# Performance work log

Hardware: AMD Instinct MI355X
Metric: run time of the kernel (lower is better)

Reference implementation:

```python
import jax, jax.numpy as jnp
import numpy as np

DT_MIN, DT_MAX = 1e-3, 0.1
DT_RANK, D_STATE, D_CONV = 64, 16, 4


def setup_inputs() -> dict:
    key = jax.random.key(0)
    ks = jax.random.split(key, 8)
    B, T, Dm = 4, 4096, 1024
    Dn = 2 * Dm  # expand * d_model
    s = lambda k, shape, scale=0.02: (jax.random.normal(k, shape, jnp.float32) * scale)
    return {
        "x": jax.random.normal(ks[0], (B, T, Dm), jnp.float32),
        "W_in": s(ks[1], (2 * Dn, Dm)),
        "conv_w": s(ks[2], (Dn, 1, D_CONV), 0.1),
        "conv_b": jnp.zeros((Dn,), jnp.float32),
        "W_x": s(ks[3], (DT_RANK + 2 * D_STATE, Dn)),
        "W_dt": s(ks[4], (Dn, DT_RANK)),
        "b_dt": jnp.zeros((Dn,), jnp.float32),
        "log_A": jax.random.uniform(ks[5], (Dn, D_STATE), jnp.float32),
        "D_param": jnp.ones((Dn,), jnp.float32),
        "W_out": s(ks[6], (Dm, Dn)),
        "ln_w": jnp.ones((Dm,), jnp.float32),
        "ln_b": jnp.zeros((Dm,), jnp.float32),
    }


def reference(x, W_in, conv_w, conv_b, W_x, W_dt, b_dt, log_A, D_param, W_out, ln_w, ln_b):
    B, T, Dm = x.shape
    Dn = W_dt.shape[0]
    residual = x
    # LayerNorm (biased variance, eps=1e-5, as torch)
    mu = x.mean(-1, keepdims=True)
    var = x.var(-1, keepdims=True)
    xn = (x - mu) / jnp.sqrt(var + 1e-5) * ln_w + ln_b
    # in_proj -> split into x_inner, z
    xz = xn @ W_in.T  # (B,T,2*Dn)
    x_inner, z = jnp.split(xz, 2, axis=-1)
    # causal depthwise conv (torch pads both sides d_conv-1 then slices [:T] == left-pad only)
    xc = jnp.transpose(x_inner, (0, 2, 1))  # (B,Dn,T)
    xc = jax.lax.conv_general_dilated(
        xc, conv_w, window_strides=(1,), padding=[(D_CONV - 1, 0)],
        dimension_numbers=("NCH", "OIH", "NCH"), feature_group_count=Dn)
    xc = xc + conv_b[None, :, None]
    u = jax.nn.silu(jnp.transpose(xc, (0, 2, 1)))  # (B,T,Dn)
    # input-dependent dt, B, C
    xbc = u @ W_x.T
    dt_low, B_ssm, C_ssm = jnp.split(xbc, [DT_RANK, DT_RANK + D_STATE], axis=-1)
    dt = jax.nn.softplus(dt_low @ W_dt.T + b_dt) + DT_MIN
    dt = jnp.clip(dt, DT_MIN, DT_MAX)  # (B,T,Dn)
    A = -jnp.exp(log_A)  # (Dn,N), always negative -> stable
    # selective scan: h_t = exp(dt*A)*h_{t-1} + (dt*u)*B_t ; y_t = <C_t, h_t>
    def step(h, inp):
        dt_t, u_t, B_t, C_t = inp  # (B,Dn),(B,Dn),(B,N),(B,N)
        dA = jnp.exp(dt_t[:, :, None] * A)  # (B,Dn,N)
        h = dA * h + (dt_t * u_t)[:, :, None] * B_t[:, None, :]
        y = jnp.einsum("bdn,bn->bd", h, C_t)
        return h, y

    h0 = jnp.zeros((B, Dn, D_STATE), x.dtype)
    _, ys = jax.lax.scan(
        step, h0,
        (jnp.moveaxis(dt, 1, 0), jnp.moveaxis(u, 1, 0),
         jnp.moveaxis(B_ssm, 1, 0), jnp.moveaxis(C_ssm, 1, 0)))
    y = jnp.moveaxis(ys, 0, 1)  # (B,T,Dn)
    y = y + u * D_param
    y = y * jax.nn.silu(z)
    return y @ W_out.T + residual
```

## Files before the change

kernel.cpp:

```cpp
#include <hip/hip_runtime.h>
#include <cstdint>
#include <cstddef>

#define TT 4096
#define DM 1024
#define DN 2048
#define MROWS 16384
#define NCH 64
#define CHL 64
#define SW 16
#define XBCS 128

typedef unsigned short u16;
typedef u16 ushort8_t __attribute__((ext_vector_type(8)));
typedef u16 ushort4_t __attribute__((ext_vector_type(4)));
typedef short bf16x8 __attribute__((ext_vector_type(8)));
typedef float f32x4 __attribute__((ext_vector_type(4)));

#define EXP2(x) __builtin_amdgcn_exp2f(x)
#define L2E 1.44269504f

__device__ __forceinline__ float bf2f(u16 b) {
  return __uint_as_float(((unsigned int)b) << 16);
}
__device__ __forceinline__ u16 f2bf(float f) {
  unsigned int u = __float_as_uint(f);
  u = u + 0x7FFFu + ((u >> 16) & 1u);
  return (u16)(u >> 16);
}
__device__ __forceinline__ u16 f2h(float f) {
  _Float16 h = (_Float16)f;
  return __builtin_bit_cast(u16, h);
}
__device__ __forceinline__ float h2f(u16 v) {
  return (float)__builtin_bit_cast(_Float16, v);
}

__device__ __forceinline__ void gload_lds16(const void* g, void* l) {
  __builtin_amdgcn_global_load_lds(
      (const __attribute__((address_space(1))) unsigned int*)g,
      (__attribute__((address_space(3))) unsigned int*)l, 16, 0, 0);
}

__global__ __launch_bounds__(256) void cvt_bf16_kernel(const float* __restrict__ in,
    u16* __restrict__ out, int n4) {
  int i = blockIdx.x * 256 + threadIdx.x;
  if (i >= n4) return;
  float4 v = ((const float4*)in)[i];
  ushort4_t o; o[0] = f2bf(v.x); o[1] = f2bf(v.y); o[2] = f2bf(v.z); o[3] = f2bf(v.w);
  ((ushort4_t*)out)[i] = o;
}

__global__ __launch_bounds__(256) void cvt_wx_kernel(const float* __restrict__ W_x,
    u16* __restrict__ out) {
  int i = blockIdx.x * 256 + threadIdx.x;
  int row = i >> 9;
  ushort4_t o;
  if (row < 96) {
    float4 v = ((const float4*)W_x)[i];
    o[0] = f2bf(v.x); o[1] = f2bf(v.y); o[2] = f2bf(v.z); o[3] = f2bf(v.w);
  } else {
    o[0] = 0; o[1] = 0; o[2] = 0; o[3] = 0;
  }
  ((ushort4_t*)out)[i] = o;
}

__global__ __launch_bounds__(256) void ln_kernel(const float* __restrict__ x,
    const float* __restrict__ ln_w, const float* __restrict__ ln_b,
    u16* __restrict__ xn) {
  int row = blockIdx.x;
  int tid = threadIdx.x;
  const float4* xr = (const float4*)(x + (size_t)row * DM);
  float4 v = xr[tid];
  float s  = v.x + v.y + v.z + v.w;
  float s2 = v.x*v.x + v.y*v.y + v.z*v.z + v.w*v.w;
#pragma unroll
  for (int o = 32; o > 0; o >>= 1) { s += __shfl_down(s, o, 64); s2 += __shfl_down(s2, o, 64); }
  __shared__ float red[2][4];
  __shared__ float mv[2];
  int wid = tid >> 6, lane = tid & 63;
  if (lane == 0) { red[0][wid] = s; red[1][wid] = s2; }
  __syncthreads();
  if (tid == 0) {
    float a  = red[0][0] + red[0][1] + red[0][2] + red[0][3];
    float b2 = red[1][0] + red[1][1] + red[1][2] + red[1][3];
    float mean = a * (1.f / DM);
    float var  = b2 * (1.f / DM) - mean * mean;
    mv[0] = mean; mv[1] = rsqrtf(var + 1e-5f);
  }
  __syncthreads();
  float mean = mv[0], inv = mv[1];
  float4 w = ((const float4*)ln_w)[tid];
  float4 b = ((const float4*)ln_b)[tid];
  ushort4_t o;
  o[0] = f2bf((v.x - mean) * inv * w.x + b.x);
  o[1] = f2bf((v.y - mean) * inv * w.y + b.y);
  o[2] = f2bf((v.z - mean) * inv * w.z + b.z);
  o[3] = f2bf((v.w - mean) * inv * w.w + b.w);
  *(ushort4_t*)(xn + (size_t)row * DM + tid * 4) = o;
}

template<int MODE>
__global__ __launch_bounds__(256) void gemm_mfma_nt(
    const u16* __restrict__ A, int lda,
    const u16* __restrict__ B, int ldb,
    void* __restrict__ Cp, int ldc,
    const float* __restrict__ Res, int K,
    const float* __restrict__ bias, u16* __restrict__ dl_out) {
  __shared__ __align__(16) u16 a_s[128 * 64];
  __shared__ __align__(16) u16 b_s[128 * 64];
  const int tid = threadIdx.x;
  const int w = tid >> 6, l = tid & 63;
  const int wr = w >> 1, wc = w & 1;
  const int nbx = gridDim.x, gy = gridDim.y;
  int lin = blockIdx.y * nbx + blockIdx.x;
  int xcd = lin & 7;
  int m   = lin >> 3;
  int bi, bj;
  if (gy >= 8) {
    int njx = gy >> 3;
    bi = m / njx;
    bj = xcd * njx + m % njx;
  } else {
    int cpx = (nbx * gy) >> 3;
    int swz = xcd * cpx + m;
    bi = swz % nbx; bj = swz / nbx;
  }
  const int lrow = l >> 3;
  const int scol = ((l & 7) ^ lrow) * 16;

  f32x4 acc[4][4] = {};

  const u16* Abase = A + (size_t)(bi * 128 + w * 8 + lrow) * lda;
  const u16* Bbase = B + (size_t)(bj * 128 + w * 8 + lrow) * ldb;

  for (int k0 = 0; k0 < K; k0 += 64) {
#pragma unroll
    for (int c = 0; c < 4; c++) {
      const char* ga = (const char*)(Abase + (size_t)(c * 32) * lda + k0) + scol;
      const char* gb = (const char*)(Bbase + (size_t)(c * 32) * ldb + k0) + scol;
      gload_lds16(ga, (char*)a_s + c * 4096 + w * 1024);
      gload_lds16(gb, (char*)b_s + c * 4096 + w * 1024);
    }
    __syncthreads();
#pragma unroll
    for (int kk = 0; kk < 2; kk++) {
      bf16x8 af[4], bfr[4];
#pragma unroll
      for (int m2 = 0; m2 < 4; m2++) {
        int fr = wr * 64 + m2 * 16 + (l & 15);
        int cb = (kk * 64 + ((l >> 4) << 4)) ^ ((fr & 7) << 4);
        af[m2] = *(const bf16x8*)((const char*)a_s + fr * 128 + cb);
      }
#pragma unroll
      for (int n = 0; n < 4; n++) {
        int fr = wc * 64 + n * 16 + (l & 15);
        int cb = (kk * 64 + ((l >> 4) << 4)) ^ ((fr & 7) << 4);
        bfr[n] = *(const bf16x8*)((const char*)b_s + fr * 128 + cb);
      }
#pragma unroll
      for (int m2 = 0; m2 < 4; m2++)
#pragma unroll
        for (int n = 0; n < 4; n++)
          acc[m2][n] = __builtin_amdgcn_mfma_f32_16x16x32_bf16(af[m2], bfr[n], acc[m2][n], 0, 0, 0);
    }
    __syncthreads();
  }
  const int col0 = bj * 128 + wc * 64 + (l & 15);
  const int row0 = bi * 128 + wr * 64 + (l >> 4) * 4;
#pragma unroll
  for (int m2 = 0; m2 < 4; m2++)
#pragma unroll
    for (int n = 0; n < 4; n++) {
      int col = col0 + n * 16;
      float bv = 0.f;
      if constexpr (MODE == 3) bv = bias[col];
#pragma unroll
      for (int r = 0; r < 4; r++) {
        size_t row = (size_t)(row0 + m2 * 16 + r);
        float v = acc[m2][n][r];
        if constexpr (MODE == 0) {
          ((u16*)Cp)[row * ldc + col] = f2bf(v);
        } else if constexpr (MODE == 1) {
          ((float*)Cp)[row * ldc + col] = v;
          if (col < 64) dl_out[row * 64 + col] = f2bf(v);
        } else if constexpr (MODE == 2) {
          v += Res[row * ldc + col];
          ((float*)Cp)[row * ldc + col] = v;
        } else {
          float s = v + bv;
          float sp = __logf(1.f + __expf(s));
          float dtv = fminf(sp + 1e-3f, 0.1f);
          ((u16*)Cp)[row * ldc + col] = f2h(dtv);
        }
      }
    }
}

__global__ __launch_bounds__(256) void conv_silu_kernel(const u16* __restrict__ xz,
    const float* __restrict__ conv_w, const float* __restrict__ conv_b,
    u16* __restrict__ u) {
  size_t gid = (size_t)blockIdx.x * 256 + threadIdx.x;
  int c = (int)(gid & 255);
  size_t i = gid >> 8;
  int t = (int)(i & (TT - 1));
  int d0 = c * 8;
  const u16* base = xz + i * 4096 + d0;
  ushort8_t r0 = *(const ushort8_t*)base;
  ushort8_t r1 = 0, r2 = 0, r3 = 0;
  if (t >= 1) r1 = *(const ushort8_t*)(base - 4096);
  if (t >= 2) r2 = *(const ushort8_t*)(base - 2 * 4096);
  if (t >= 3) r3 = *(const ushort8_t*)(base - 3 * 4096);
  float cbv[8];
  *(float4*)&cbv[0] = *(const float4*)(conv_b + d0);
  *(float4*)&cbv[4] = *(const float4*)(conv_b + d0 + 4);
  ushort8_t o;
#pragma unroll
  for (int j = 0; j < 8; j++) {
    float4 w = *(const float4*)(conv_w + (size_t)(d0 + j) * 4);
    float a = cbv[j] + w.w * bf2f(r0[j]) + w.z * bf2f(r1[j])
            + w.y * bf2f(r2[j]) + w.x * bf2f(r3[j]);
    a = a * __builtin_amdgcn_rcpf(1.f + EXP2(-a * L2E));
    o[j] = f2bf(a);
  }
  *(ushort8_t*)(u + i * 2048 + d0) = o;
}

__global__ __launch_bounds__(256) void scan_part1(u16* u_g,
    const u16* __restrict__ dt_g, const float* __restrict__ xbc,
    const float* __restrict__ log_A, const float* __restrict__ D_param,
    float* __restrict__ hbuf, float* __restrict__ Sbuf) {
  int d0 = blockIdx.x * 128;
  int c  = blockIdx.y;
  int b  = blockIdx.z;
  int tid = threadIdx.x;
  int w = tid >> 6, l = tid & 63;
  int dl = tid >> 1, q = tid & 1, q8 = q << 3;
  int d = d0 + dl;
  __shared__ __align__(16) u16 u_s[2][SW][128];
  __shared__ __align__(16) u16 dts[2][SW][128];
  __shared__ __align__(16) float bc_s[2][SW][32];

  float A2[8];
  {
    float4 la0 = *(const float4*)(log_A + (size_t)d * 16 + q8);
    float4 la1 = *(const float4*)(log_A + (size_t)d * 16 + q8 + 4);
    A2[0] = -EXP2(la0.x * L2E) * L2E; A2[1] = -EXP2(la0.y * L2E) * L2E;
    A2[2] = -EXP2(la0.z * L2E) * L2E; A2[3] = -EXP2(la0.w * L2E) * L2E;
    A2[4] = -EXP2(la1.x * L2E) * L2E; A2[5] = -EXP2(la1.y * L2E) * L2E;
    A2[6] = -EXP2(la1.z * L2E) * L2E; A2[7] = -EXP2(la1.w * L2E) * L2E;
  }
  float Dp = D_param[d];
  float h[8] = {};
  float sdt = 0.f;
  size_t t0 = (size_t)b * TT + (size_t)c * CHL;
  const int sr = w * 4 + (l >> 4);
  const int sc = (l & 15) * 8;
  u16* up = u_g + t0 * 2048 + d;

#define P1STAGE(wnd, pb) { size_t i0_ = t0 + (size_t)(wnd) * SW;                          \
    gload_lds16(u_g  + (i0_ + sr) * 2048 + d0 + sc, (char*)u_s[pb] + w * 1024);           \
    gload_lds16(dt_g + (i0_ + sr) * 4096 + d0 + sc, (char*)dts[pb] + w * 1024);           \
    if (w < 2) gload_lds16(xbc + (i0_ + w * 8 + (l >> 3)) * XBCS + 64 + (l & 7) * 4,      \
                           (char*)bc_s[pb] + w * 1024); }

  P1STAGE(0, 0);
  for (int wnd = 0; wnd < CHL / SW; wnd++) {
    int pb = wnd & 1;
    __syncthreads();
    if (wnd + 1 < CHL / SW) P1STAGE(wnd + 1, pb ^ 1);
#pragma unroll 4
    for (int tt = 0; tt < SW; tt++) {
      float dtv = h2f(dts[pb][tt][dl]);
      float uv  = bf2f(u_s[pb][tt][dl]);
      sdt += dtv;
      float xin = dtv * uv;
      float yv = q ? 0.f : uv * Dp;
      float4 B0 = *(const float4*)&bc_s[pb][tt][q8];
      float4 B1 = *(const float4*)&bc_s[pb][tt][q8 + 4];
      float4 C0 = *(const float4*)&bc_s[pb][tt][16 + q8];
      float4 C1 = *(const float4*)&bc_s[pb][tt][16 + q8 + 4];
      h[0] = __builtin_fmaf(EXP2(dtv * A2[0]), h[0], xin * B0.x); yv = __builtin_fmaf(h[0], C0.x, yv);
      h[1] = __builtin_fmaf(EXP2(dtv * A2[1]), h[1], xin * B0.y); yv = __builtin_fmaf(h[1], C0.y, yv);
      h[2] = __builtin_fmaf(EXP2(dtv * A2[2]), h[2], xin * B0.z); yv = __builtin_fmaf(h[2], C0.z, yv);
      h[3] = __builtin_fmaf(EXP2(dtv * A2[3]), h[3], xin * B0.w); yv = __builtin_fmaf(h[3], C0.w, yv);
      h[4] = __builtin_fmaf(EXP2(dtv * A2[4]), h[4], xin * B1.x); yv = __builtin_fmaf(h[4], C1.x, yv);
      h[5] = __builtin_fmaf(EXP2(dtv * A2[5]), h[5], xin * B1.y); yv = __builtin_fmaf(h[5], C1.y, yv);
      h[6] = __builtin_fmaf(EXP2(dtv * A2[6]), h[6], xin * B1.z); yv = __builtin_fmaf(h[6], C1.z, yv);
      h[7] = __builtin_fmaf(EXP2(dtv * A2[7]), h[7], xin * B1.w); yv = __builtin_fmaf(h[7], C1.w, yv);
      yv += __shfl_xor(yv, 1, 64);
      if (q == 0) *up = f2h(yv);
      up += 2048;
    }
  }
  float* hp = hbuf + (((size_t)b * NCH + c) * 16 + q8) * DN + d;
#pragma unroll
  for (int k = 0; k < 8; k++) hp[(size_t)k * DN] = h[k];
  if (q == 0) Sbuf[((size_t)b * NCH + c) * DN + d] = sdt;
#undef P1STAGE
}

__global__ __launch_bounds__(256) void scan_combine(const float* __restrict__ log_A,
    const float* __restrict__ Sbuf, float* __restrict__ hbuf) {
  int idx = blockIdx.x * 256 + threadIdx.x;
  int dd = idx & (DN - 1), n = (idx >> 11) & 15, b = idx >> 15;
  float A2 = -EXP2(log_A[(size_t)dd * 16 + n] * L2E) * L2E;
  float h = 0.f;
#pragma unroll
  for (int c = 0; c < NCH; c++) {
    size_t off = (((size_t)b * NCH + c) * 16 + n) * DN + dd;
    float hl = hbuf[off];
    float P = EXP2(A2 * Sbuf[((size_t)b * NCH + c) * DN + dd]);
    hbuf[off] = h;
    h = hl + P * h;
  }
}

__global__ __launch_bounds__(256) void scan_part2(u16* yl,
    const u16* __restrict__ xz, const float* __restrict__ xbc,
    const u16* __restrict__ dt_g, const float* __restrict__ log_A,
    const float* __restrict__ hbuf) {
  int d0 = blockIdx.x * 128;
  int c  = blockIdx.y;
  int b  = blockIdx.z;
  int tid = threadIdx.x;
  int w = tid >> 6, l = tid & 63;
  int dl = tid >> 1, q = tid & 1, q8 = q << 3;
  int d = d0 + dl;
  __shared__ __align__(16) u16 yls[2][SW][128];
  __shared__ __align__(16) u16 z_s[2][SW][128];
  __shared__ __align__(16) u16 dts[2][SW][128];
  __shared__ __align__(16) float c_s[2][SW][16];

  float A2[8];
  {
    float4 la0 = *(const float4*)(log_A + (size_t)d * 16 + q8);
    float4 la1 = *(const float4*)(log_A + (size_t)d * 16 + q8 + 4);
    A2[0] = -EXP2(la0.x * L2E) * L2E; A2[1] = -EXP2(la0.y * L2E) * L2E;
    A2[2] = -EXP2(la0.z * L2E) * L2E; A2[3] = -EXP2(la0.w * L2E) * L2E;
    A2[4] = -EXP2(la1.x * L2E) * L2E; A2[5] = -EXP2(la1.y * L2E) * L2E;
    A2[6] = -EXP2(la1.z * L2E) * L2E; A2[7] = -EXP2(la1.w * L2E) * L2E;
  }
  float hs[8];
  {
    const float* hp = hbuf + (((size_t)b * NCH + c) * 16 + q8) * DN + d;
#pragma unroll
    for (int k = 0; k < 8; k++) hs[k] = hp[(size_t)k * DN];
  }
  float cum = 0.f;
  size_t t0 = (size_t)b * TT + (size_t)c * CHL;
  const int sr = w * 4 + (l >> 4);
  const int sc = (l & 15) * 8;
  u16* ylp = yl + t0 * 2048 + d;

#define P2STAGE(wnd, pb) { size_t i0_ = t0 + (size_t)(wnd) * SW;                          \
    gload_lds16(yl   + (i0_ + sr) * 2048 + d0 + sc, (char*)yls[pb] + w * 1024);           \
    gload_lds16(xz   + (i0_ + sr) * 4096 + 2048 + d0 + sc, (char*)z_s[pb] + w * 1024);    \
    gload_lds16(dt_g + (i0_ + sr) * 4096 + d0 + sc, (char*)dts[pb] + w * 1024);           \
    if (w == 0) gload_lds16(xbc + (i0_ + (l >> 2)) * XBCS + 80 + (l & 3) * 4,             \
                            (char*)c_s[pb]); }

  P2STAGE(0, 0);
  for (int wnd = 0; wnd < CHL / SW; wnd++) {
    int pb = wnd & 1;
    __syncthreads();
    if (wnd + 1 < CHL / SW) P2STAGE(wnd + 1, pb ^ 1);
#pragma unroll 4
    for (int tt = 0; tt < SW; tt++) {
      float dtv = h2f(dts[pb][tt][dl]);
      cum += dtv;
      float4 C0 = *(const float4*)&c_s[pb][tt][q8];
      float4 C1 = *(const float4*)&c_s[pb][tt][q8 + 4];
      float yv = C0.x * (EXP2(cum * A2[0]) * hs[0]) + C0.y * (EXP2(cum * A2[1]) * hs[1])
               + C0.z * (EXP2(cum * A2[2]) * hs[2]) + C0.w * (EXP2(cum * A2[3]) * hs[3])
               + C1.x * (EXP2(cum * A2[4]) * hs[4]) + C1.y * (EXP2(cum * A2[5]) * hs[5])
               + C1.z * (EXP2(cum * A2[6]) * hs[6]) + C1.w * (EXP2(cum * A2[7]) * hs[7]);
      if (q == 0) yv += h2f(yls[pb][tt][dl]);
      yv += __shfl_xor(yv, 1, 64);
      float zv = bf2f(z_s[pb][tt][dl]);
      float sig = __builtin_amdgcn_rcpf(1.f + EXP2(-zv * L2E));
      if (q == 0) *ylp = f2bf(yv * zv * sig);
      ylp += 2048;
    }
  }
#undef P2STAGE
}

extern "C" void kernel_launch(void* const* d_in, const int* in_sizes, int n_in,
                              void* d_out, int out_size, void* d_ws, size_t ws_size,
                              hipStream_t stream) {
  const float* x       = (const float*)d_in[0];
  const float* W_in    = (const float*)d_in[1];
  const float* conv_w  = (const float*)d_in[2];
  const float* conv_b  = (const float*)d_in[3];
  const float* W_x     = (const float*)d_in[4];
  const float* W_dt    = (const float*)d_in[5];
  const float* b_dt    = (const float*)d_in[6];
  const float* log_A   = (const float*)d_in[7];
  const float* D_param = (const float*)d_in[8];
  const float* W_out   = (const float*)d_in[9];
  const float* ln_w    = (const float*)d_in[10];
  const float* ln_b    = (const float*)d_in[11];
  float* out = (float*)d_out;

  size_t need = (size_t)MROWS * 4096 * 2 + (size_t)MROWS * DN * 2 + (size_t)MROWS * 96 * 4;
  if (ws_size < need) return;
  u16*   xz  = (u16*)d_ws;
  u16*   u   = xz + (size_t)MROWS * 4096;
  u16*   W_out_b = (u16*)(u + (size_t)MROWS * DN);

  u16*   xn_b    = (u16*)d_out;
  float* xbc     = (float*)d_out;
  float* hbuf    = (float*)((char*)d_out + (8u << 20));
  u16*   W_in_b  = (u16*)((char*)d_out + (40u << 20));
  float* Sbuf    = (float*)((char*)d_out + (48u << 20));
  u16*   W_x_b   = (u16*)((char*)d_out + (50u << 20));
  u16*   W_dt_b  = (u16*)((char*)d_out + (50u << 20) + (512u << 10));
  u16*   dl_b    = (u16*)((char*)d_out + (51u << 20));

  cvt_wx_kernel<<<(128 * 2048 / 4) / 256, 256, 0, stream>>>(W_x, W_x_b);
  cvt_bf16_kernel<<<(2048 * 64 / 4) / 256, 256, 0, stream>>>(W_dt, W_dt_b, 2048 * 64 / 4);
  ln_kernel<<<MROWS, 256, 0, stream>>>(x, ln_w, ln_b, xn_b);
  cvt_bf16_kernel<<<(4096 * 1024 / 4) / 256, 256, 0, stream>>>(W_in, W_in_b, 4096 * 1024 / 4);
  gemm_mfma_nt<0><<<dim3(MROWS / 128, 4096 / 128), 256, 0, stream>>>(
      xn_b, DM, W_in_b, DM, xz, 4096, nullptr, DM, nullptr, nullptr);
  conv_silu_kernel<<<MROWS, 256, 0, stream>>>(xz, conv_w, conv_b, u);
  gemm_mfma_nt<1><<<dim3(MROWS / 128, XBCS / 128), 256, 0, stream>>>(
      u, DN, W_x_b, DN, xbc, XBCS, nullptr, DN, nullptr, dl_b);
  gemm_mfma_nt<3><<<dim3(MROWS / 128, DN / 128), 256, 0, stream>>>(
      dl_b, 64, W_dt_b, 64, xz, 4096, nullptr, 64, b_dt, nullptr);
  scan_part1<<<dim3(DN / 128, NCH, 4), 256, 0, stream>>>(
      u, xz, xbc, log_A, D_param, hbuf, Sbuf);
  scan_combine<<<4 * DN * 16 / 256, 256, 0, stream>>>(log_A, Sbuf, hbuf);
  scan_part2<<<dim3(DN / 128, NCH, 4), 256, 0, stream>>>(
      u, xz, xbc, xz, log_A, hbuf);
  cvt_bf16_kernel<<<(1024 * 2048 / 4) / 256, 256, 0, stream>>>(W_out, W_out_b, 1024 * 2048 / 4);
  gemm_mfma_nt<2><<<dim3(MROWS / 128, 1024 / 128), 256, 0, stream>>>(
      u, DN, W_out_b, DN, out, DM, x, DN, nullptr, nullptr);
}
```

Before: 665.4 us.

## Add 256x256-tile 512-thread MFMA GEMM with interleaved prefetch for in/out projections

Adds a new GEMM kernel using 256x256 block tiles, 8 waves, double-buffered 128KB dynamic LDS and finely interleaved global-to-LDS prefetches with MFMA groups, explicit vmcnt waits and s_setprio. It replaces the 128x128 kernel for the large in_proj and out_proj GEMMs to raise arithmetic intensity per byte loaded and overlap loads with compute. Risks include low occupancy from large LDS use, and fewer blocks for the out_proj GEMM (64x4 = 256 tiles), which may underfill the GPU. A fallback to the old kernel runs if the LDS attribute cannot be set.

```diff
diff --git a/kernel.cpp b/kernel.cpp
--- a/kernel.cpp
+++ b/kernel.cpp
@@ -41,6 +41,8 @@
       (const __attribute__((address_space(1))) unsigned int*)g,
       (__attribute__((address_space(3))) unsigned int*)l, 16, 0, 0);
 }
+
+#define FENCE() asm volatile("" ::: "memory")
 
 __global__ __launch_bounds__(256) void cvt_bf16_kernel(const float* __restrict__ in,
     u16* __restrict__ out, int n4) {
@@ -115,7 +117,7 @@
   const int nbx = gridDim.x, gy = gridDim.y;
   int lin = blockIdx.y * nbx + blockIdx.x;
   int xcd = lin & 7;
-  int m   = lin >> 3;
+  int m = lin >> 3;
   int bi, bj;
   if (gy >= 8) {
     int njx = gy >> 3;
@@ -192,6 +194,122 @@
           float sp = __logf(1.f + __expf(s));
           float dtv = fminf(sp + 1e-3f, 0.1f);
           ((u16*)Cp)[row * ldc + col] = f2h(dtv);
+        }
+      }
+    }
+}
+
+template<int MODE>
+__global__ __launch_bounds__(512) void gemm256(
+    const u16* __restrict__ A, int lda,
+    const u16* __restrict__ B, int ldb,
+    void* __restrict__ Cp, int ldc,
+    const float* __restrict__ Res, int K) {
+  extern __shared__ char smem[];
+  const int tid = threadIdx.x;
+  const int w = tid >> 6, l = tid & 63;
+  const int wm = w >> 2, wn = w & 3;
+  const int nbx = gridDim.x, gy = gridDim.y;
+  int lin = blockIdx.y * nbx + blockIdx.x;
+  int xcd = lin & 7, mm = lin >> 3;
+  int bi, bj;
+  if (gy >= 8) { int njx = gy >> 3; bi = mm / njx; bj = xcd * njx + mm % njx; }
+  else { int cpx = (nbx * gy) >> 3; int swz = xcd * cpx + mm; bi = swz % nbx; bj = swz / nbx; }
+  const int lrow = l >> 3;
+  const int scol = ((l & 7) ^ lrow) * 16;
+  const int l15 = l & 15, lhi = (l >> 4) << 4;
+  const u16* aRow = A + (size_t)(bi * 256 + w * 8 + lrow) * lda;
+  const u16* bRow = B + (size_t)(bj * 256 + w * 8 + lrow) * ldb;
+  char* As = smem;
+  char* Bs = smem + 65536;
+
+#define IS_A(s, k) gload_lds16((const char*)(aRow + (size_t)((k) * 64) * lda + (size_t)(s) * 64) + scol, \
+                               As + ((((s) & 1)) << 15) + (k) * 8192 + w * 1024)
+#define IS_B(s, k) gload_lds16((const char*)(bRow + (size_t)((k) * 64) * ldb + (size_t)(s) * 64) + scol, \
+                               Bs + ((((s) & 1)) << 15) + (k) * 8192 + w * 1024)
+
+  f32x4 acc[8][4] = {};
+  bf16x8 bf[2][4];
+  const int NT = K >> 6;
+
+  IS_B(0, 0); IS_B(0, 1); IS_B(0, 2); IS_B(0, 3);
+  IS_A(0, 0); IS_A(0, 2); IS_A(0, 1); IS_A(0, 3);
+  IS_B(1, 0); IS_B(1, 1); IS_B(1, 2); IS_B(1, 3); IS_A(1, 0);
+
+#define MFMA8(MLO, KK) do { \
+    bf16x8 a0_ = ardA(MLO, KK), a1_ = ardA((MLO) + 1, KK); \
+    __builtin_amdgcn_s_setprio(1); \
+    _Pragma("unroll") \
+    for (int n_ = 0; n_ < 4; n_++) { \
+      acc[MLO][n_]       = __builtin_amdgcn_mfma_f32_16x16x32_bf16(a0_, bf[KK][n_], acc[MLO][n_], 0, 0, 0); \
+      acc[(MLO) + 1][n_] = __builtin_amdgcn_mfma_f32_16x16x32_bf16(a1_, bf[KK][n_], acc[(MLO) + 1][n_], 0, 0, 0); \
+    } \
+    __builtin_amdgcn_s_setprio(0); \
+  } while (0)
+
+  for (int t = 0; t < NT; ++t) {
+    const char* Ab = As + ((t & 1) << 15);
+    const char* Bb = Bs + ((t & 1) << 15);
+    auto ardA = [&](int m, int kk) {
+      int fr = wm * 128 + m * 16 + l15;
+      int cb = (kk * 64 + lhi) ^ ((fr & 7) << 4);
+      return *(const bf16x8*)(Ab + fr * 128 + cb);
+    };
+    auto ardB = [&](int n, int kk) {
+      int fr = wn * 64 + n * 16 + l15;
+      int cb = (kk * 64 + lhi) ^ ((fr & 7) << 4);
+      return *(const bf16x8*)(Bb + fr * 128 + cb);
+    };
+    if (t + 1 < NT) IS_A(t + 1, 2);
+    FENCE();
+    asm volatile("s_waitcnt vmcnt(8)" ::: "memory");
+    __builtin_amdgcn_s_barrier();
+    FENCE();
+    bf[0][0] = ardB(0, 0); bf[0][1] = ardB(1, 0); bf[0][2] = ardB(2, 0); bf[0][3] = ardB(3, 0);
+    MFMA8(0, 0);
+    if (t + 1 < NT) IS_A(t + 1, 1);
+    MFMA8(2, 0);
+    if (t + 1 < NT) IS_A(t + 1, 3);
+    bf[1][0] = ardB(0, 1); bf[1][1] = ardB(1, 1); bf[1][2] = ardB(2, 1); bf[1][3] = ardB(3, 1);
+    MFMA8(0, 1);
+    FENCE();
+    __builtin_amdgcn_s_barrier();
+    FENCE();
+    if (t + 2 < NT) IS_B(t + 2, 0);
+    MFMA8(2, 1);
+    if (t + 2 < NT) IS_B(t + 2, 1);
+    FENCE();
+    asm volatile("s_waitcnt vmcnt(10)" ::: "memory");
+    __builtin_amdgcn_s_barrier();
+    FENCE();
+    MFMA8(4, 0);
+    if (t + 2 < NT) IS_B(t + 2, 2);
+    MFMA8(6, 0);
+    if (t + 2 < NT) IS_B(t + 2, 3);
+    MFMA8(4, 1);
+    if (t + 2 < NT) IS_A(t + 2, 0);
+    MFMA8(6, 1);
+  }
+#undef MFMA8
+#undef IS_A
+#undef IS_B
+
+  const int col0 = bj * 256 + wn * 64 + l15;
+  const int row0 = bi * 256 + wm * 128 + (l >> 4) * 4;
+#pragma unroll
+  for (int m = 0; m < 8; m++)
+#pragma unroll
+    for (int n = 0; n < 4; n++) {
+      int col = col0 + n * 16;
+#pragma unroll
+      for (int r = 0; r < 4; r++) {
+        size_t row = (size_t)(row0 + m * 16 + r);
+        float v = acc[m][n][r];
+        if constexpr (MODE == 0) {
+          ((u16*)Cp)[row * ldc + col] = f2bf(v);
+        } else {
+          v += Res[row * ldc + col];
+          ((float*)Cp)[row * ldc + col] = v;
         }
       }
     }
@@ -418,12 +536,26 @@
   u16*   W_dt_b  = (u16*)((char*)d_out + (50u << 20) + (512u << 10));
   u16*   dl_b    = (u16*)((char*)d_out + (51u << 20));
 
+  static int use256 = -1;
+  if (use256 < 0) {
+    hipError_t e0 = hipFuncSetAttribute(reinterpret_cast<const void*>(&gemm256<0>),
+        hipFuncAttributeMaxDynamicSharedMemorySize, 131072);
+    hipError_t e2 = hipFuncSetAttribute(reinterpret_cast<const void*>(&gemm256<2>),
+        hipFuncAttributeMaxDynamicSharedMemorySize, 131072);
+    use256 = (e0 == hipSuccess && e2 == hipSuccess) ? 1 : 0;
+  }
+
   cvt_wx_kernel<<<(128 * 2048 / 4) / 256, 256, 0, stream>>>(W_x, W_x_b);
   cvt_bf16_kernel<<<(2048 * 64 / 4) / 256, 256, 0, stream>>>(W_dt, W_dt_b, 2048 * 64 / 4);
   ln_kernel<<<MROWS, 256, 0, stream>>>(x, ln_w, ln_b, xn_b);
   cvt_bf16_kernel<<<(4096 * 1024 / 4) / 256, 256, 0, stream>>>(W_in, W_in_b, 4096 * 1024 / 4);
-  gemm_mfma_nt<0><<<dim3(MROWS / 128, 4096 / 128), 256, 0, stream>>>(
-      xn_b, DM, W_in_b, DM, xz, 4096, nullptr, DM, nullptr, nullptr);
+  if (use256) {
+    gemm256<0><<<dim3(MROWS / 256, 4096 / 256), 512, 131072, stream>>>(
+        xn_b, DM, W_in_b, DM, xz, 4096, nullptr, DM);
+  } else {
+    gemm_mfma_nt<0><<<dim3(MROWS / 128, 4096 / 128), 256, 0, stream>>>(
+        xn_b, DM, W_in_b, DM, xz, 4096, nullptr, DM, nullptr, nullptr);
+  }
   conv_silu_kernel<<<MROWS, 256, 0, stream>>>(xz, conv_w, conv_b, u);
   gemm_mfma_nt<1><<<dim3(MROWS / 128, XBCS / 128), 256, 0, stream>>>(
       u, DN, W_x_b, DN, xbc, XBCS, nullptr, DN, nullptr, dl_b);
@@ -435,6 +567,11 @@
   scan_part2<<<dim3(DN / 128, NCH, 4), 256, 0, stream>>>(
       u, xz, xbc, xz, log_A, hbuf);
   cvt_bf16_kernel<<<(1024 * 2048 / 4) / 256, 256, 0, stream>>>(W_out, W_out_b, 1024 * 2048 / 4);
-  gemm_mfma_nt<2><<<dim3(MROWS / 128, 1024 / 128), 256, 0, stream>>>(
-      u, DN, W_out_b, DN, out, DM, x, DN, nullptr, nullptr);
-}
+  if (use256) {
+    gemm256<2><<<dim3(MROWS / 256, 1024 / 256), 512, 131072, stream>>>(
+        u, DN, W_out_b, DN, out, DM, x, DN);
+  } else {
+    gemm_mfma_nt<2><<<dim3(MROWS / 128, 1024 / 128), 256, 0, stream>>>(
+        u, DN, W_out_b, DN, out, DM, x, DN, nullptr, nullptr);
+  }
+}
```

Result: faster. 623.5 us (-6.3%).
